# Kernel optimization log

Measured on AMD Instinct MI355X. Metric: run time of the kernel, lower is better.

Reference implementation:

```python
import jax, jax.numpy as jnp
import numpy as np

N = 50000
E = 800000
D_IN = 128
D_OUT = 128


def setup_inputs() -> dict:
    key = jax.random.key(0)
    ks = jax.random.split(key, 12)
    x = jax.random.normal(ks[0], (N, D_IN), dtype=jnp.float32)
    W1 = jax.random.normal(ks[1], (D_IN, D_OUT), dtype=jnp.float32) * (1.0 / np.sqrt(D_IN))
    b1 = jnp.zeros((D_OUT,), dtype=jnp.float32)
    W2 = jax.random.normal(ks[2], (D_IN, D_OUT), dtype=jnp.float32) * (1.0 / np.sqrt(D_IN))
    b2 = jnp.zeros((D_OUT,), dtype=jnp.float32)
    # inverted-dropout masks, p=0.5 -> values in {0, 2}
    def mask(k):
        return jnp.where(jax.random.uniform(k, (N, D_IN)) < 0.5, 0.0, 2.0).astype(jnp.float32)
    mask_pos1 = mask(ks[3])
    mask_neg1 = mask(ks[4])
    mask_pos2 = mask(ks[5])
    mask_neg2 = mask(ks[6])
    edge_index1 = jax.random.randint(ks[7], (2, E), 0, N, dtype=jnp.int32)
    edge_index2 = jax.random.randint(ks[8], (2, E), 0, N, dtype=jnp.int32)
    perm1 = jax.random.permutation(ks[9], N).astype(jnp.int32)
    perm2 = jax.random.permutation(ks[10], N).astype(jnp.int32)
    return dict(x=x, W1=W1, b1=b1, W2=W2, b2=b2,
                mask_pos1=mask_pos1, mask_neg1=mask_neg1,
                mask_pos2=mask_pos2, mask_neg2=mask_neg2,
                edge_index1=edge_index1, edge_index2=edge_index2,
                perm1=perm1, perm2=perm2)


def gcn_conv(x, W, b, edge_index):
    """PyG GCNConv: add self-loops, symmetric normalization, then x@W aggregation + bias."""
    n = x.shape[0]
    xw = x @ W  # [N, D_OUT]
    loops = jnp.arange(n, dtype=edge_index.dtype)
    src = jnp.concatenate([edge_index[0], loops])
    dst = jnp.concatenate([edge_index[1], loops])
    deg = jax.ops.segment_sum(jnp.ones_like(dst, dtype=xw.dtype), dst, num_segments=n)
    dinv = jax.lax.rsqrt(jnp.maximum(deg, 1.0))  # deg >= 1 due to self-loops
    norm = dinv[src] * dinv[dst]                 # [E+N]
    msg = xw[src] * norm[:, None]                # [E+N, D_OUT]
    out = jax.ops.segment_sum(msg, dst, num_segments=n)
    return out + b


def _branch(x, W, b, edge_index, mask_pos, mask_neg, perm):
    pos_h = jax.nn.relu(gcn_conv(x * mask_pos, W, b, edge_index))
    neg_in = (x * mask_neg)[perm]
    neg_h = jax.nn.relu(gcn_conv(neg_in, W, b, edge_index))
    summary = jnp.mean(pos_h, axis=0, keepdims=True)  # [1, D_OUT]
    return pos_h, neg_h, summary


def reference(x, W1, b1, W2, b2, mask_pos1, mask_neg1, mask_pos2, mask_neg2,
              edge_index1, edge_index2, perm1, perm2):
    p1, n1, s1 = _branch(x, W1, b1, edge_index1, mask_pos1, mask_neg1, perm1)
    p2, n2, s2 = _branch(x, W2, b2, edge_index2, mask_pos2, mask_neg2, perm2)
    return (p1, n1, s1, p2, n2, s2)
```

## Files before the change

kernel.cpp:

```cpp
#include <hip/hip_runtime.h>
#include <hip/hip_fp16.h>

#define NN 50000
#define NE 800000
#define D 128
#define FILL_BLOCKS 1024
#define GEMM_BLOCKS 3128
#define NBKT 64
#define BW 782
#define BCAP 16384

typedef _Float16 half8_t __attribute__((ext_vector_type(8)));
typedef _Float16 half4_t __attribute__((ext_vector_type(4)));
typedef float f32x4 __attribute__((ext_vector_type(4)));

__global__ void k_init(float* s1, float* s2, int* bcnt) {
    int i = threadIdx.x;
    if (i < D) { s1[i] = 0.f; s2[i] = 0.f; }
    if (i < 2 * NBKT) bcnt[i] = 0;
}

__global__ void k_bucket(const int* __restrict__ src1, const int* __restrict__ dst1,
                         const int* __restrict__ src2, const int* __restrict__ dst2,
                         int* bcnt,
                         int* bs1, int* bd1, int* bs2, int* bd2) {
    __shared__ int lcnt[128], lpos[128], gbase[128];
    int t = threadIdx.x;
    if (t < 128) { lcnt[t] = 0; lpos[t] = 0; }
    __syncthreads();

    int e0 = blockIdx.x * 256 + t;
    int s1v0=0,d1v0=0,s2v0=0,d2v0=0, s1v1=0,d1v1=0,s2v1=0,d2v1=0;
    int s1v2=0,d1v2=0,s2v2=0,d2v2=0, s1v3=0,d1v3=0,s2v3=0,d2v3=0;
    bool v0 = (e0 + 0 * 262144) < NE;
    bool v1 = (e0 + 1 * 262144) < NE;
    bool v2 = (e0 + 2 * 262144) < NE;
    bool v3 = (e0 + 3 * 262144) < NE;
    if (v0) { int e = e0;             s1v0 = src1[e]; d1v0 = dst1[e]; s2v0 = src2[e]; d2v0 = dst2[e]; }
    if (v1) { int e = e0 + 262144;    s1v1 = src1[e]; d1v1 = dst1[e]; s2v1 = src2[e]; d2v1 = dst2[e]; }
    if (v2) { int e = e0 + 2*262144;  s1v2 = src1[e]; d1v2 = dst1[e]; s2v2 = src2[e]; d2v2 = dst2[e]; }
    if (v3) { int e = e0 + 3*262144;  s1v3 = src1[e]; d1v3 = dst1[e]; s2v3 = src2[e]; d2v3 = dst2[e]; }

    if (v0) { atomicAdd(&lcnt[d1v0 / BW], 1); atomicAdd(&lcnt[NBKT + d2v0 / BW], 1); }
    if (v1) { atomicAdd(&lcnt[d1v1 / BW], 1); atomicAdd(&lcnt[NBKT + d2v1 / BW], 1); }
    if (v2) { atomicAdd(&lcnt[d1v2 / BW], 1); atomicAdd(&lcnt[NBKT + d2v2 / BW], 1); }
    if (v3) { atomicAdd(&lcnt[d1v3 / BW], 1); atomicAdd(&lcnt[NBKT + d2v3 / BW], 1); }
    __syncthreads();
    if (t < 128) gbase[t] = atomicAdd(&bcnt[t], lcnt[t]);
    __syncthreads();

    #define PLACE(sv, dv) { \
        int r = (dv) / BW; \
        int p = gbase[r] + atomicAdd(&lpos[r], 1); \
        if (p < BCAP) { bs1[r * BCAP + p] = (sv); bd1[r * BCAP + p] = (dv); } }
    #define PLACE2(sv, dv) { \
        int r = (dv) / BW; \
        int p = gbase[NBKT + r] + atomicAdd(&lpos[NBKT + r], 1); \
        if (p < BCAP) { bs2[r * BCAP + p] = (sv); bd2[r * BCAP + p] = (dv); } }
    if (v0) { PLACE(s1v0, d1v0); PLACE2(s2v0, d2v0); }
    if (v1) { PLACE(s1v1, d1v1); PLACE2(s2v1, d2v1); }
    if (v2) { PLACE(s1v2, d1v2); PLACE2(s2v2, d2v2); }
    if (v3) { PLACE(s1v3, d1v3); PLACE2(s2v3, d2v3); }
    #undef PLACE
    #undef PLACE2
}

__global__ void k_hist(const int* __restrict__ bcnt,
                       const int* __restrict__ bd1, const int* __restrict__ bd2,
                       int* rp1, int* rp2, int* cur1, int* cur2,
                       float* dinv1, float* dinv2) {
    __shared__ int h[1024];
    __shared__ int tsum[256];
    __shared__ int tb[64];
    __shared__ int bbase;
    int t = threadIdx.x;
    int g = blockIdx.x >> 6;
    int f = blockIdx.x & 63;
    const int* bd = g ? bd2 : bd1;
    int* rp = g ? rp2 : rp1;
    int* cur = g ? cur2 : cur1;
    float* dinv = g ? dinv2 : dinv1;
    int n = bcnt[g * NBKT + f];
    if (n > BCAP) n = BCAP;

    h[t] = 0; h[t + 256] = 0; h[t + 512] = 0; h[t + 768] = 0;
    if (t < NBKT) tb[t] = bcnt[g * NBKT + t];
    __syncthreads();

    const int* bdf = bd + f * BCAP;
    for (int i = t; i < n; i += 256) atomicAdd(&h[bdf[i] - f * BW], 1);
    if (t == 0) { int b = 0; for (int j = 0; j < f; j++) b += tb[j]; bbase = b; }
    __syncthreads();

    int a0 = h[4*t], a1 = h[4*t+1], a2 = h[4*t+2], a3 = h[4*t+3];
    int s = a0 + a1 + a2 + a3;
    tsum[t] = s;
    __syncthreads();
    for (int off = 1; off < 256; off <<= 1) {
        int add = (t >= off) ? tsum[t - off] : 0;
        __syncthreads();
        tsum[t] += add;
        __syncthreads();
    }
    int excl = tsum[t] - s + bbase;

    int idx = 4 * t;
    int gd = f * BW + idx;
    int e0 = excl, e1 = excl + a0, e2 = excl + a0 + a1, e3 = excl + a0 + a1 + a2;
    if (idx + 0 < BW && gd + 0 < NN) { rp[gd+0] = e0; cur[gd+0] = e0; dinv[gd+0] = rsqrtf((float)(a0+1)); }
    if (idx + 1 < BW && gd + 1 < NN) { rp[gd+1] = e1; cur[gd+1] = e1; dinv[gd+1] = rsqrtf((float)(a1+1)); }
    if (idx + 2 < BW && gd + 2 < NN) { rp[gd+2] = e2; cur[gd+2] = e2; dinv[gd+2] = rsqrtf((float)(a2+1)); }
    if (idx + 3 < BW && gd + 3 < NN) { rp[gd+3] = e3; cur[gd+3] = e3; dinv[gd+3] = rsqrtf((float)(a3+1)); }
    if (f == 63 && t == 0) rp[NN] = NE;
}

__launch_bounds__(256)
__global__ void k_fill_gemm(const int* __restrict__ bcnt,
                            const int* __restrict__ bs1, const int* __restrict__ bd1,
                            const int* __restrict__ bs2, const int* __restrict__ bd2,
                            int* cur1, int* cur2, int* col1, int* col2,
                            const float* __restrict__ x,
                            const float* __restrict__ W1, const float* __restrict__ W2,
                            const float* __restrict__ mp1, const float* __restrict__ mn1,
                            const float* __restrict__ mp2, const float* __restrict__ mn2,
                            const int* __restrict__ perm1, const int* __restrict__ perm2,
                            const float* __restrict__ dinv1, const float* __restrict__ dinv2,
                            _Float16* xwi1, _Float16* xwi2) {
    __shared__ __align__(16) _Float16 WT[128][136];
    int t = threadIdx.x;
    int bid = blockIdx.x;

    if (bid < FILL_BLOCKS) {
        int f = (bid & 7) + 8 * ((bid >> 3) & 7);
        int rank = bid >> 6;
        int base = f * BCAP;
        int n1 = bcnt[f];         if (n1 > BCAP) n1 = BCAP;
        int n2 = bcnt[NBKT + f];  if (n2 > BCAP) n2 = BCAP;
        for (int i = rank * 256 + t; i < n1; i += 4096) {
            int d = bd1[base + i];
            int p = atomicAdd(&cur1[d], 1);
            col1[p] = bs1[base + i];
        }
        for (int i = rank * 256 + t; i < n2; i += 4096) {
            int d = bd2[base + i];
            int p = atomicAdd(&cur2[d], 1);
            col2[p] = bs2[base + i];
        }
        return;
    }

    int g = bid - FILL_BLOCKS;
    int which = g / 782;
    int bx = g - which * 782;
    const float* W = (which < 2) ? W1 : W2;
    const float* mask = (which == 0) ? mp1 : (which == 1) ? mn1 : (which == 2) ? mp2 : mn2;
    const int* perm = (which == 1) ? perm1 : (which == 3) ? perm2 : nullptr;
    const float* dinv = (which < 2) ? dinv1 : dinv2;
    _Float16* out = ((which < 2) ? xwi1 : xwi2) + ((which & 1) ? 128 : 0);

    #pragma unroll
    for (int i = 0; i < 8; i++) {
        int idx = i * 256 + t;
        int j = idx & 127;
        int k0 = (idx >> 7) * 8;
        half8_t h;
        #pragma unroll
        for (int c = 0; c < 8; c++) h[c] = (_Float16)W[(k0 + c) * 128 + j];
        *(half8_t*)(&WT[j][k0]) = h;
    }
    __syncthreads();

    int wave = t >> 6;
    int lane = t & 63;
    int quad = lane >> 4;
    int m = lane & 15;
    int tile = bx * 4 + wave;
    bool active = (tile * 16 < NN);

    f32x4 accs[8];
    if (active) {
        int row = tile * 16 + m;
        int grow = perm ? perm[row] : row;
        const float* xrow = x + (long)grow * D;
        const float* mrow = mask + (long)grow * D;

        half8_t a[4];
        #pragma unroll
        for (int kk = 0; kk < 4; kk++) {
            int k0 = kk * 32 + quad * 8;
            float4 xa = *(const float4*)(xrow + k0);
            float4 xb = *(const float4*)(xrow + k0 + 4);
            float4 ma = *(const float4*)(mrow + k0);
            float4 mb = *(const float4*)(mrow + k0 + 4);
            a[kk][0] = (_Float16)(xa.x * ma.x);
            a[kk][1] = (_Float16)(xa.y * ma.y);
            a[kk][2] = (_Float16)(xa.z * ma.z);
            a[kk][3] = (_Float16)(xa.w * ma.w);
            a[kk][4] = (_Float16)(xb.x * mb.x);
            a[kk][5] = (_Float16)(xb.y * mb.y);
            a[kk][6] = (_Float16)(xb.z * mb.z);
            a[kk][7] = (_Float16)(xb.w * mb.w);
        }

        #pragma unroll
        for (int nt = 0; nt < 8; nt++) {
            f32x4 acc = {0.f, 0.f, 0.f, 0.f};
            #pragma unroll
            for (int kk = 0; kk < 4; kk++) {
                half8_t w = *(const half8_t*)(&WT[nt * 16 + m][kk * 32 + quad * 8]);
                acc = __builtin_amdgcn_mfma_f32_16x16x32_f16(w, a[kk], acc, 0, 0, 0);
            }
            accs[nt] = acc;
        }
    }

    __syncthreads();

    if (active) {
        float ds = dinv[tile * 16 + m];
        _Float16* st = &WT[0][0] + wave * 2176;

        #pragma unroll
        for (int nt = 0; nt < 8; nt++) {
            half4_t h;
            h[0] = (_Float16)(accs[nt][0] * ds);
            h[1] = (_Float16)(accs[nt][1] * ds);
            h[2] = (_Float16)(accs[nt][2] * ds);
            h[3] = (_Float16)(accs[nt][3] * ds);
            *(half4_t*)(st + m * 136 + nt * 16 + quad * 4) = h;
        }
        #pragma unroll
        for (int p = 0; p < 4; p++) {
            int r = lane & 15;
            int cc = (lane >> 4) + p * 4;
            half8_t v = *(const half8_t*)(st + r * 136 + cc * 8);
            *(half8_t*)(out + (long)(tile * 16 + r) * 256 + cc * 8) = v;
        }
    }
}

__launch_bounds__(256)
__global__ void k_agg(const _Float16* __restrict__ xwi1, const _Float16* __restrict__ xwi2,
                      const int* __restrict__ rp1, const int* __restrict__ col1,
                      const float* __restrict__ dinv1,
                      const int* __restrict__ rp2, const int* __restrict__ col2,
                      const float* __restrict__ dinv2,
                      const float* __restrict__ b1, const float* __restrict__ b2,
                      float* out) {
    int g = blockIdx.y;
    const _Float16* xwi = g ? xwi2 : xwi1;
    const int* rp = g ? rp2 : rp1;
    const int* col = g ? col2 : col1;
    const float* dinv = g ? dinv2 : dinv1;
    const float* bias = g ? b2 : b1;
    float* pos_out = out + (g ? 12800128L : 0L);
    float* neg_out = out + (g ? 19200128L : 6400000L);

    int t = threadIdx.x;
    int wave = t >> 6, lane = t & 63;
    int i = blockIdx.x * 4 + wave;
    if (i >= NN) return;
    int j4 = lane * 4;

    half4_t sv = *(const half4_t*)(xwi + (long)i * 256 + j4);
    float a0 = (float)sv[0], a1 = (float)sv[1], a2 = (float)sv[2], a3 = (float)sv[3];
    int e0 = rp[i], e1 = rp[i + 1];
    int e = e0;
    for (; e + 8 <= e1; e += 8) {
        int s0 = col[e + 0], s1 = col[e + 1], s2 = col[e + 2], s3 = col[e + 3];
        int s4 = col[e + 4], s5 = col[e + 5], s6 = col[e + 6], s7 = col[e + 7];
        half4_t v0 = *(const half4_t*)(xwi + (long)s0 * 256 + j4);
        half4_t v1 = *(const half4_t*)(xwi + (long)s1 * 256 + j4);
        half4_t v2 = *(const half4_t*)(xwi + (long)s2 * 256 + j4);
        half4_t v3 = *(const half4_t*)(xwi + (long)s3 * 256 + j4);
        half4_t v4 = *(const half4_t*)(xwi + (long)s4 * 256 + j4);
        half4_t v5 = *(const half4_t*)(xwi + (long)s5 * 256 + j4);
        half4_t v6 = *(const half4_t*)(xwi + (long)s6 * 256 + j4);
        half4_t v7 = *(const half4_t*)(xwi + (long)s7 * 256 + j4);
        a0 += (float)v0[0] + (float)v1[0] + (float)v2[0] + (float)v3[0]
            + (float)v4[0] + (float)v5[0] + (float)v6[0] + (float)v7[0];
        a1 += (float)v0[1] + (float)v1[1] + (float)v2[1] + (float)v3[1]
            + (float)v4[1] + (float)v5[1] + (float)v6[1] + (float)v7[1];
        a2 += (float)v0[2] + (float)v1[2] + (float)v2[2] + (float)v3[2]
            + (float)v4[2] + (float)v5[2] + (float)v6[2] + (float)v7[2];
        a3 += (float)v0[3] + (float)v1[3] + (float)v2[3] + (float)v3[3]
            + (float)v4[3] + (float)v5[3] + (float)v6[3] + (float)v7[3];
    }
    for (; e + 4 <= e1; e += 4) {
        int s0 = col[e + 0], s1 = col[e + 1], s2 = col[e + 2], s3 = col[e + 3];
        half4_t v0 = *(const half4_t*)(xwi + (long)s0 * 256 + j4);
        half4_t v1 = *(const half4_t*)(xwi + (long)s1 * 256 + j4);
        half4_t v2 = *(const half4_t*)(xwi + (long)s2 * 256 + j4);
        half4_t v3 = *(const half4_t*)(xwi + (long)s3 * 256 + j4);
        a0 += (float)v0[0] + (float)v1[0] + (float)v2[0] + (float)v3[0];
        a1 += (float)v0[1] + (float)v1[1] + (float)v2[1] + (float)v3[1];
        a2 += (float)v0[2] + (float)v1[2] + (float)v2[2] + (float)v3[2];
        a3 += (float)v0[3] + (float)v1[3] + (float)v2[3] + (float)v3[3];
    }
    for (; e < e1; e++) {
        int s = col[e];
        half4_t v = *(const half4_t*)(xwi + (long)s * 256 + j4);
        a0 += (float)v[0]; a1 += (float)v[1]; a2 += (float)v[2]; a3 += (float)v[3];
    }
    float di = dinv[i];
    int jj = (lane < 32) ? j4 : (j4 - 128);
    const f32x4* bp = (const f32x4*)(bias + jj);
    f32x4 bv = *bp;
    f32x4 o;
    o[0] = fmaxf(0.f, di * a0 + bv[0]);
    o[1] = fmaxf(0.f, di * a1 + bv[1]);
    o[2] = fmaxf(0.f, di * a2 + bv[2]);
    o[3] = fmaxf(0.f, di * a3 + bv[3]);
    float* dst = ((lane < 32) ? pos_out : neg_out) + (long)i * D + jj;
    __builtin_nontemporal_store(o, (f32x4*)dst);
}

__launch_bounds__(256)
__global__ void k_sum(const float* __restrict__ pos1, const float* __restrict__ pos2,
                      float* s1, float* s2) {
    int g = blockIdx.y;
    const float* pos = g ? pos2 : pos1;
    float* s = g ? s2 : s1;
    int t = threadIdx.x;
    int rg = t >> 5;
    int j = (t & 31) * 4;
    float4 acc = {0.f, 0.f, 0.f, 0.f};
    for (int i = blockIdx.x * 8 + rg; i < NN; i += gridDim.x * 8) {
        float4 v = *(const float4*)(pos + (long)i * D + j);
        acc.x += v.x; acc.y += v.y; acc.z += v.z; acc.w += v.w;
    }
    __shared__ float sm[8][128];
    sm[rg][j + 0] = acc.x;
    sm[rg][j + 1] = acc.y;
    sm[rg][j + 2] = acc.z;
    sm[rg][j + 3] = acc.w;
    __syncthreads();
    if (t < 128) {
        float v = 0.f;
        for (int r = 0; r < 8; r++) v += sm[r][t];
        atomicAdd(&s[t], v * (1.0f / NN));
    }
}

extern "C" void kernel_launch(void* const* d_in, const int* in_sizes, int n_in,
                              void* d_out, int out_size, void* d_ws, size_t ws_size,
                              hipStream_t stream) {
    const float* x   = (const float*)d_in[0];
    const float* W1  = (const float*)d_in[1];
    const float* b1  = (const float*)d_in[2];
    const float* W2  = (const float*)d_in[3];
    const float* b2  = (const float*)d_in[4];
    const float* mp1 = (const float*)d_in[5];
    const float* mn1 = (const float*)d_in[6];
    const float* mp2 = (const float*)d_in[7];
    const float* mn2 = (const float*)d_in[8];
    const int* e1 = (const int*)d_in[9];
    const int* e2 = (const int*)d_in[10];
    const int* perm1 = (const int*)d_in[11];
    const int* perm2 = (const int*)d_in[12];
    const int* src1 = e1;       const int* dst1 = e1 + NE;
    const int* src2 = e2;       const int* dst2 = e2 + NE;
    float* out = (float*)d_out;

    char* w = (char*)d_ws;
    _Float16* xwi1 = (_Float16*)w; w += (size_t)NN * 256 * 2;
    _Float16* xwi2 = (_Float16*)w; w += (size_t)NN * 256 * 2;
    int* cur1 = (int*)w;  w += (size_t)NN * 4;
    int* cur2 = (int*)w;  w += (size_t)NN * 4;
    int* rp1 = (int*)w;   w += (size_t)(NN + 4) * 4;
    int* rp2 = (int*)w;   w += (size_t)(NN + 4) * 4;
    int* col1 = (int*)w;  w += (size_t)NE * 4;
    int* col2 = (int*)w;  w += (size_t)NE * 4;
    float* dinv1 = (float*)w; w += (size_t)NN * 4;
    float* dinv2 = (float*)w; w += (size_t)NN * 4;
    int* bcnt  = (int*)w; w += (size_t)128 * 4;
    int* bs1 = (int*)w;   w += (size_t)NBKT * BCAP * 4;
    int* bd1 = (int*)w;   w += (size_t)NBKT * BCAP * 4;
    int* bs2 = (int*)w;   w += (size_t)NBKT * BCAP * 4;
    int* bd2 = (int*)w;   w += (size_t)NBKT * BCAP * 4;

    float* s1 = out + 12800000L;
    float* s2 = out + 25600128L;
    const float* pos1 = out;
    const float* pos2 = out + 12800128L;

    k_init<<<dim3(1), 256, 0, stream>>>(s1, s2, bcnt);
    k_bucket<<<dim3(1024), 256, 0, stream>>>(src1, dst1, src2, dst2, bcnt,
                                             bs1, bd1, bs2, bd2);
    k_hist<<<dim3(128), 256, 0, stream>>>(bcnt, bd1, bd2,
                                          rp1, rp2, cur1, cur2, dinv1, dinv2);
    k_fill_gemm<<<dim3(FILL_BLOCKS + GEMM_BLOCKS), 256, 0, stream>>>(
        bcnt, bs1, bd1, bs2, bd2, cur1, cur2, col1, col2,
        x, W1, W2, mp1, mn1, mp2, mn2, perm1, perm2, dinv1, dinv2, xwi1, xwi2);
    k_agg<<<dim3(12500, 2), 256, 0, stream>>>(xwi1, xwi2,
                                              rp1, col1, dinv1, rp2, col2, dinv2,
                                              b1, b2, out);
    k_sum<<<dim3(128, 2), 256, 0, stream>>>(pos1, pos2, s1, s2);
}
```

Before: 475.4 us.

## Fuse CSR fill into histogram kernel with shared cursors; pretranspose W once

The CSR column fill moves out of the combined fill+GEMM kernel into the histogram kernel, now 512 threads per bucket. It keeps per-destination cursors in shared memory instead of using global atomics on a cursor array, which removes the cur arrays and their global atomic traffic. W1 and W2 are transposed and cast to fp16 once in the init kernel. The GEMM then reads W fragments straight from global/L2 instead of having every block rebuild a transposed tile in LDS. The trade-off is that the fill can no longer overlap with the GEMM blocks, and only 128 blocks do the fill work.

```diff
diff --git a/kernel.cpp b/kernel.cpp
--- a/kernel.cpp
+++ b/kernel.cpp
@@ -4,7 +4,6 @@
 #define NN 50000
 #define NE 800000
 #define D 128
-#define FILL_BLOCKS 1024
 #define GEMM_BLOCKS 3128
 #define NBKT 64
 #define BW 782
@@ -14,10 +13,15 @@
 typedef _Float16 half4_t __attribute__((ext_vector_type(4)));
 typedef float f32x4 __attribute__((ext_vector_type(4)));
 
-__global__ void k_init(float* s1, float* s2, int* bcnt) {
-    int i = threadIdx.x;
+__global__ void k_init(float* s1, float* s2, int* bcnt,
+                       const float* __restrict__ W1, const float* __restrict__ W2,
+                       _Float16* wt1, _Float16* wt2) {
+    int i = blockIdx.x * 256 + threadIdx.x;
     if (i < D) { s1[i] = 0.f; s2[i] = 0.f; }
     if (i < 2 * NBKT) bcnt[i] = 0;
+    int n = i >> 7, k = i & 127;
+    wt1[n * 128 + k] = (_Float16)W1[k * 128 + n];
+    wt2[n * 128 + k] = (_Float16)W2[k * 128 + n];
 }
 
 __global__ void k_bucket(const int* __restrict__ src1, const int* __restrict__ dst1,
@@ -65,177 +69,141 @@
     #undef PLACE2
 }
 
-__global__ void k_hist(const int* __restrict__ bcnt,
-                       const int* __restrict__ bd1, const int* __restrict__ bd2,
-                       int* rp1, int* rp2, int* cur1, int* cur2,
-                       float* dinv1, float* dinv2) {
+__launch_bounds__(512)
+__global__ void k_build(const int* __restrict__ bcnt,
+                        const int* __restrict__ bs1, const int* __restrict__ bd1,
+                        const int* __restrict__ bs2, const int* __restrict__ bd2,
+                        int* rp1, int* rp2, int* col1, int* col2,
+                        float* dinv1, float* dinv2) {
     __shared__ int h[1024];
-    __shared__ int tsum[256];
+    __shared__ int tsum[512];
     __shared__ int tb[64];
     __shared__ int bbase;
     int t = threadIdx.x;
     int g = blockIdx.x >> 6;
     int f = blockIdx.x & 63;
-    const int* bd = g ? bd2 : bd1;
+    const int* bd = (g ? bd2 : bd1) + f * BCAP;
+    const int* bs = (g ? bs2 : bs1) + f * BCAP;
     int* rp = g ? rp2 : rp1;
-    int* cur = g ? cur2 : cur1;
+    int* col = g ? col2 : col1;
     float* dinv = g ? dinv2 : dinv1;
     int n = bcnt[g * NBKT + f];
     if (n > BCAP) n = BCAP;
 
-    h[t] = 0; h[t + 256] = 0; h[t + 512] = 0; h[t + 768] = 0;
+    h[t] = 0; h[t + 512] = 0;
     if (t < NBKT) tb[t] = bcnt[g * NBKT + t];
     __syncthreads();
 
-    const int* bdf = bd + f * BCAP;
-    for (int i = t; i < n; i += 256) atomicAdd(&h[bdf[i] - f * BW], 1);
+    for (int i = t; i < n; i += 512) atomicAdd(&h[bd[i] - f * BW], 1);
+    __syncthreads();
     if (t == 0) { int b = 0; for (int j = 0; j < f; j++) b += tb[j]; bbase = b; }
-    __syncthreads();
-
-    int a0 = h[4*t], a1 = h[4*t+1], a2 = h[4*t+2], a3 = h[4*t+3];
-    int s = a0 + a1 + a2 + a3;
+
+    int a0 = h[2 * t], a1 = h[2 * t + 1];
+    int s = a0 + a1;
     tsum[t] = s;
     __syncthreads();
-    for (int off = 1; off < 256; off <<= 1) {
+    for (int off = 1; off < 512; off <<= 1) {
         int add = (t >= off) ? tsum[t - off] : 0;
         __syncthreads();
         tsum[t] += add;
         __syncthreads();
     }
     int excl = tsum[t] - s + bbase;
-
-    int idx = 4 * t;
-    int gd = f * BW + idx;
-    int e0 = excl, e1 = excl + a0, e2 = excl + a0 + a1, e3 = excl + a0 + a1 + a2;
-    if (idx + 0 < BW && gd + 0 < NN) { rp[gd+0] = e0; cur[gd+0] = e0; dinv[gd+0] = rsqrtf((float)(a0+1)); }
-    if (idx + 1 < BW && gd + 1 < NN) { rp[gd+1] = e1; cur[gd+1] = e1; dinv[gd+1] = rsqrtf((float)(a1+1)); }
-    if (idx + 2 < BW && gd + 2 < NN) { rp[gd+2] = e2; cur[gd+2] = e2; dinv[gd+2] = rsqrtf((float)(a2+1)); }
-    if (idx + 3 < BW && gd + 3 < NN) { rp[gd+3] = e3; cur[gd+3] = e3; dinv[gd+3] = rsqrtf((float)(a3+1)); }
+    int idx = 2 * t, gd = f * BW + idx;
+    int e0 = excl, e1 = excl + a0;
+    h[2 * t] = e0; h[2 * t + 1] = e1;
+    if (idx < BW && gd < NN)         { rp[gd]     = e0; dinv[gd]     = rsqrtf((float)(a0 + 1)); }
+    if (idx + 1 < BW && gd + 1 < NN) { rp[gd + 1] = e1; dinv[gd + 1] = rsqrtf((float)(a1 + 1)); }
     if (f == 63 && t == 0) rp[NN] = NE;
+    __syncthreads();
+
+    for (int i = t; i < n; i += 512) {
+        int p = atomicAdd(&h[bd[i] - f * BW], 1);
+        col[p] = bs[i];
+    }
 }
 
 __launch_bounds__(256)
-__global__ void k_fill_gemm(const int* __restrict__ bcnt,
-                            const int* __restrict__ bs1, const int* __restrict__ bd1,
-                            const int* __restrict__ bs2, const int* __restrict__ bd2,
-                            int* cur1, int* cur2, int* col1, int* col2,
-                            const float* __restrict__ x,
-                            const float* __restrict__ W1, const float* __restrict__ W2,
-                            const float* __restrict__ mp1, const float* __restrict__ mn1,
-                            const float* __restrict__ mp2, const float* __restrict__ mn2,
-                            const int* __restrict__ perm1, const int* __restrict__ perm2,
-                            const float* __restrict__ dinv1, const float* __restrict__ dinv2,
-                            _Float16* xwi1, _Float16* xwi2) {
-    __shared__ __align__(16) _Float16 WT[128][136];
-    int t = threadIdx.x;
-    int bid = blockIdx.x;
-
-    if (bid < FILL_BLOCKS) {
-        int f = (bid & 7) + 8 * ((bid >> 3) & 7);
-        int rank = bid >> 6;
-        int base = f * BCAP;
-        int n1 = bcnt[f];         if (n1 > BCAP) n1 = BCAP;
-        int n2 = bcnt[NBKT + f];  if (n2 > BCAP) n2 = BCAP;
-        for (int i = rank * 256 + t; i < n1; i += 4096) {
-            int d = bd1[base + i];
-            int p = atomicAdd(&cur1[d], 1);
-            col1[p] = bs1[base + i];
-        }
-        for (int i = rank * 256 + t; i < n2; i += 4096) {
-            int d = bd2[base + i];
-            int p = atomicAdd(&cur2[d], 1);
-            col2[p] = bs2[base + i];
-        }
-        return;
-    }
-
-    int g = bid - FILL_BLOCKS;
+__global__ void k_gemm(const _Float16* __restrict__ wt1, const _Float16* __restrict__ wt2,
+                       const float* __restrict__ x,
+                       const float* __restrict__ mp1, const float* __restrict__ mn1,
+                       const float* __restrict__ mp2, const float* __restrict__ mn2,
+                       const int* __restrict__ perm1, const int* __restrict__ perm2,
+                       const float* __restrict__ dinv1, const float* __restrict__ dinv2,
+                       _Float16* xwi1, _Float16* xwi2) {
+    __shared__ __align__(16) _Float16 ST[4][16][136];
+
+    int g = blockIdx.x;
     int which = g / 782;
     int bx = g - which * 782;
-    const float* W = (which < 2) ? W1 : W2;
+    const _Float16* wt = (which < 2) ? wt1 : wt2;
     const float* mask = (which == 0) ? mp1 : (which == 1) ? mn1 : (which == 2) ? mp2 : mn2;
     const int* perm = (which == 1) ? perm1 : (which == 3) ? perm2 : nullptr;
     const float* dinv = (which < 2) ? dinv1 : dinv2;
     _Float16* out = ((which < 2) ? xwi1 : xwi2) + ((which & 1) ? 128 : 0);
 
-    #pragma unroll
-    for (int i = 0; i < 8; i++) {
-        int idx = i * 256 + t;
-        int j = idx & 127;
-        int k0 = (idx >> 7) * 8;
-        half8_t h;
-        #pragma unroll
-        for (int c = 0; c < 8; c++) h[c] = (_Float16)W[(k0 + c) * 128 + j];
-        *(half8_t*)(&WT[j][k0]) = h;
-    }
-    __syncthreads();
-
+    int t = threadIdx.x;
     int wave = t >> 6;
     int lane = t & 63;
     int quad = lane >> 4;
     int m = lane & 15;
     int tile = bx * 4 + wave;
-    bool active = (tile * 16 < NN);
+    if (tile * 16 >= NN) return;
+
+    int row = tile * 16 + m;
+    int grow = perm ? perm[row] : row;
+    const float* xrow = x + (long)grow * D;
+    const float* mrow = mask + (long)grow * D;
+
+    half8_t a[4];
+    #pragma unroll
+    for (int kk = 0; kk < 4; kk++) {
+        int k0 = kk * 32 + quad * 8;
+        float4 xa = *(const float4*)(xrow + k0);
+        float4 xb = *(const float4*)(xrow + k0 + 4);
+        float4 ma = *(const float4*)(mrow + k0);
+        float4 mb = *(const float4*)(mrow + k0 + 4);
+        a[kk][0] = (_Float16)(xa.x * ma.x);
+        a[kk][1] = (_Float16)(xa.y * ma.y);
+        a[kk][2] = (_Float16)(xa.z * ma.z);
+        a[kk][3] = (_Float16)(xa.w * ma.w);
+        a[kk][4] = (_Float16)(xb.x * mb.x);
+        a[kk][5] = (_Float16)(xb.y * mb.y);
+        a[kk][6] = (_Float16)(xb.z * mb.z);
+        a[kk][7] = (_Float16)(xb.w * mb.w);
+    }
 
     f32x4 accs[8];
-    if (active) {
-        int row = tile * 16 + m;
-        int grow = perm ? perm[row] : row;
-        const float* xrow = x + (long)grow * D;
-        const float* mrow = mask + (long)grow * D;
-
-        half8_t a[4];
+    #pragma unroll
+    for (int nt = 0; nt < 8; nt++) {
+        const _Float16* wrow = wt + (nt * 16 + m) * 128 + quad * 8;
+        f32x4 acc = {0.f, 0.f, 0.f, 0.f};
         #pragma unroll
         for (int kk = 0; kk < 4; kk++) {
-            int k0 = kk * 32 + quad * 8;
-            float4 xa = *(const float4*)(xrow + k0);
-            float4 xb = *(const float4*)(xrow + k0 + 4);
-            float4 ma = *(const float4*)(mrow + k0);
-            float4 mb = *(const float4*)(mrow + k0 + 4);
-            a[kk][0] = (_Float16)(xa.x * ma.x);
-            a[kk][1] = (_Float16)(xa.y * ma.y);
-            a[kk][2] = (_Float16)(xa.z * ma.z);
-            a[kk][3] = (_Float16)(xa.w * ma.w);
-            a[kk][4] = (_Float16)(xb.x * mb.x);
-            a[kk][5] = (_Float16)(xb.y * mb.y);
-            a[kk][6] = (_Float16)(xb.z * mb.z);
-            a[kk][7] = (_Float16)(xb.w * mb.w);
+            half8_t w = *(const half8_t*)(wrow + kk * 32);
+            acc = __builtin_amdgcn_mfma_f32_16x16x32_f16(w, a[kk], acc, 0, 0, 0);
         }
-
-        #pragma unroll
-        for (int nt = 0; nt < 8; nt++) {
-            f32x4 acc = {0.f, 0.f, 0.f, 0.f};
-            #pragma unroll
-            for (int kk = 0; kk < 4; kk++) {
-                half8_t w = *(const half8_t*)(&WT[nt * 16 + m][kk * 32 + quad * 8]);
-                acc = __builtin_amdgcn_mfma_f32_16x16x32_f16(w, a[kk], acc, 0, 0, 0);
-            }
-            accs[nt] = acc;
-        }
-    }
-
-    __syncthreads();
-
-    if (active) {
-        float ds = dinv[tile * 16 + m];
-        _Float16* st = &WT[0][0] + wave * 2176;
-
-        #pragma unroll
-        for (int nt = 0; nt < 8; nt++) {
-            half4_t h;
-            h[0] = (_Float16)(accs[nt][0] * ds);
-            h[1] = (_Float16)(accs[nt][1] * ds);
-            h[2] = (_Float16)(accs[nt][2] * ds);
-            h[3] = (_Float16)(accs[nt][3] * ds);
-            *(half4_t*)(st + m * 136 + nt * 16 + quad * 4) = h;
-        }
-        #pragma unroll
-        for (int p = 0; p < 4; p++) {
-            int r = lane & 15;
-            int cc = (lane >> 4) + p * 4;
-            half8_t v = *(const half8_t*)(st + r * 136 + cc * 8);
-            *(half8_t*)(out + (long)(tile * 16 + r) * 256 + cc * 8) = v;
-        }
+        accs[nt] = acc;
+    }
+
+    float ds = dinv[tile * 16 + m];
+    _Float16* st = &ST[wave][0][0];
+
+    #pragma unroll
+    for (int nt = 0; nt < 8; nt++) {
+        half4_t h;
+        h[0] = (_Float16)(accs[nt][0] * ds);
+        h[1] = (_Float16)(accs[nt][1] * ds);
+        h[2] = (_Float16)(accs[nt][2] * ds);
+        h[3] = (_Float16)(accs[nt][3] * ds);
+        *(half4_t*)(st + m * 136 + nt * 16 + quad * 4) = h;
+    }
+    #pragma unroll
+    for (int p = 0; p < 4; p++) {
+        int r = lane & 15;
+        int cc = (lane >> 4) + p * 4;
+        half8_t v = *(const half8_t*)(st + r * 136 + cc * 8);
+        *(half8_t*)(out + (long)(tile * 16 + r) * 256 + cc * 8) = v;
     }
 }
 
@@ -365,8 +333,6 @@
     char* w = (char*)d_ws;
     _Float16* xwi1 = (_Float16*)w; w += (size_t)NN * 256 * 2;
     _Float16* xwi2 = (_Float16*)w; w += (size_t)NN * 256 * 2;
-    int* cur1 = (int*)w;  w += (size_t)NN * 4;
-    int* cur2 = (int*)w;  w += (size_t)NN * 4;
     int* rp1 = (int*)w;   w += (size_t)(NN + 4) * 4;
     int* rp2 = (int*)w;   w += (size_t)(NN + 4) * 4;
     int* col1 = (int*)w;  w += (size_t)NE * 4;
@@ -378,20 +344,21 @@
     int* bd1 = (int*)w;   w += (size_t)NBKT * BCAP * 4;
     int* bs2 = (int*)w;   w += (size_t)NBKT * BCAP * 4;
     int* bd2 = (int*)w;   w += (size_t)NBKT * BCAP * 4;
+    _Float16* wt1 = (_Float16*)w; w += (size_t)D * D * 2;
+    _Float16* wt2 = (_Float16*)w; w += (size_t)D * D * 2;
 
     float* s1 = out + 12800000L;
     float* s2 = out + 25600128L;
     const float* pos1 = out;
     const float* pos2 = out + 12800128L;
 
-    k_init<<<dim3(1), 256, 0, stream>>>(s1, s2, bcnt);
+    k_init<<<dim3(64), 256, 0, stream>>>(s1, s2, bcnt, W1, W2, wt1, wt2);
     k_bucket<<<dim3(1024), 256, 0, stream>>>(src1, dst1, src2, dst2, bcnt,
                                              bs1, bd1, bs2, bd2);
-    k_hist<<<dim3(128), 256, 0, stream>>>(bcnt, bd1, bd2,
-                                          rp1, rp2, cur1, cur2, dinv1, dinv2);
-    k_fill_gemm<<<dim3(FILL_BLOCKS + GEMM_BLOCKS), 256, 0, stream>>>(
-        bcnt, bs1, bd1, bs2, bd2, cur1, cur2, col1, col2,
-        x, W1, W2, mp1, mn1, mp2, mn2, perm1, perm2, dinv1, dinv2, xwi1, xwi2);
+    k_build<<<dim3(128), 512, 0, stream>>>(bcnt, bs1, bd1, bs2, bd2,
+                                           rp1, rp2, col1, col2, dinv1, dinv2);
+    k_gemm<<<dim3(GEMM_BLOCKS), 256, 0, stream>>>(wt1, wt2,
+        x, mp1, mn1, mp2, mn2, perm1, perm2, dinv1, dinv2, xwi1, xwi2);
     k_agg<<<dim3(12500, 2), 256, 0, stream>>>(xwi1, xwi2,
                                               rp1, col1, dinv1, rp2, col2, dinv2,
                                               b1, b2, out);
```

New measurement: 465.6 us. -2.0%, faster.
